# Kernel tuning notes

Measured on AMD Instinct MI355X. Metric: run time of the kernel, lower is better.

The kernel has to match this reference:

```python
import jax, jax.numpy as jnp
import numpy as np

N, M, D_IN, D_OUT = 100000, 1024, 64, 64


def setup_inputs() -> dict:
    key = jax.random.key(0)
    ks = jax.random.split(key, 8)
    # kaiming_uniform_ bound for fan_in = D_IN: sqrt(6 / fan_in) with a=sqrt(5) default? torch's
    # kaiming_uniform_ default (a=0) gives bound = sqrt(6/fan_in); exact init is irrelevant for math.
    bound = float(np.sqrt(6.0 / D_IN))
    return {
        "x": jax.random.normal(ks[0], (N, D_IN), dtype=jnp.float32),
        "neighbors": jax.random.normal(ks[1], (M, D_IN), dtype=jnp.float32),
        "Wq": jax.random.uniform(ks[2], (D_OUT, D_IN), jnp.float32, -bound, bound),
        "bq": jnp.zeros((D_OUT,), jnp.float32),
        "Wk": jax.random.uniform(ks[3], (D_OUT, D_IN), jnp.float32, -bound, bound),
        "bk": jnp.zeros((D_OUT,), jnp.float32),
        "Wv": jax.random.uniform(ks[4], (D_OUT, D_IN), jnp.float32, -bound, bound),
        "bv": jnp.zeros((D_OUT,), jnp.float32),
    }


def reference(x, neighbors, Wq, bq, Wk, bk, Wv, bv):
    # q: [N, D_OUT], k: [M, D_OUT]
    q = x @ Wq.T + bq
    k = neighbors @ Wk.T + bk
    # scores: [N, M] -- same math as sum(q[:,None,:] * k[None,:,:], axis=2) but via GEMM
    scores = q @ k.T
    attn = jax.nn.softmax(scores, axis=1)
    # attn @ neighbors: [N, D_IN], then value projection -> [N, D_OUT]
    agg = attn @ neighbors
    return agg @ Wv.T + bv
```

## Files before the change

### kernel.cpp

```cpp
#include <hip/hip_runtime.h>


#define N_ROWS 100000
#define LOG2E 1.44269504088896f
#define GATE_THR 11.5424f

typedef __attribute__((ext_vector_type(8))) _Float16 half8;
typedef __attribute__((ext_vector_type(4))) float    f32x4;

#define MFMA16(a,b,c) __builtin_amdgcn_mfma_f32_16x16x32_f16((a),(b),(c),0,0,0)

static __device__ __forceinline__ f32x4 zero4() {
    f32x4 v = {0.f, 0.f, 0.f, 0.f};
    return v;
}

__global__ __launch_bounds__(256)
void prep_kernel(const float* __restrict__ nb, const float* __restrict__ Wq,
                 const float* __restrict__ bq, const float* __restrict__ Wk,
                 unsigned short* __restrict__ GFh, unsigned short* __restrict__ GFl,
                 float* __restrict__ uW, unsigned short* __restrict__ KF,
                 unsigned short* __restrict__ VF)
{
    __shared__ __align__(16) float sm[8192];
    const int tid = threadIdx.x;
    if (blockIdx.x == 0) {
        const float4* wk4 = (const float4*)Wk;
        const float4* wq4 = (const float4*)Wq;
        float4* dk = (float4*)sm;
        float4* dq = (float4*)(sm + 4096);
        #pragma unroll
        for (int u = 0; u < 4; u++) {
            dk[u * 256 + tid] = wk4[u * 256 + tid];
            dq[u * 256 + tid] = wq4[u * 256 + tid];
        }
        __syncthreads();
        const int e2 = tid & 63, e1g = (tid >> 6) * 16;
        float g[16];
        #pragma unroll
        for (int q = 0; q < 16; q++) g[q] = 0.f;
        for (int w = 0; w < 64; w++) {
            float kv = sm[w * 64 + e2];
            const float* wqp = sm + 4096 + w * 64 + e1g;
            #pragma unroll
            for (int q = 0; q < 16; q++) g[q] = fmaf(wqp[q], kv, g[q]);
        }
        union { half8 h; uint4 u; } ph0, pl0, ph1, pl1;
        #pragma unroll
        for (int i = 0; i < 8; i++) {
            _Float16 h0 = (_Float16)g[i];
            ph0.h[i] = h0; pl0.h[i] = (_Float16)(g[i] - (float)h0);
            _Float16 h1 = (_Float16)g[8 + i];
            ph1.h[i] = h1; pl1.h[i] = (_Float16)(g[8 + i] - (float)h1);
        }
        const int mt = e2 >> 4, cc = e2 & 15;
        const int ks = tid >> 7, Q0 = 2 * ((tid >> 6) & 1);
        const int f  = mt * 2 + ks;
        *(uint4*)(GFh + (f * 64 + Q0 * 16 + cc) * 8)       = ph0.u;
        *(uint4*)(GFh + (f * 64 + (Q0 + 1) * 16 + cc) * 8) = ph1.u;
        *(uint4*)(GFl + (f * 64 + Q0 * 16 + cc) * 8)       = pl0.u;
        *(uint4*)(GFl + (f * 64 + (Q0 + 1) * 16 + cc) * 8) = pl1.u;
        if (tid < 64) {
            float uu = 0.f;
            for (int w = 0; w < 64; w++) uu = fmaf(bq[w], sm[w * 64 + tid], uu);
            uW[tid] = uu;
        }
    } else {
        const int j0 = (blockIdx.x - 1) * 64;
        const int T0 = (blockIdx.x - 1) * 2;
        {
            const int jr = tid >> 2, c0 = (tid & 3) * 16;
            const float* np = nb + (size_t)(j0 + jr) * 64 + c0;
            #pragma unroll
            for (int u = 0; u < 4; u++) {
                float4 v = *(const float4*)(np + 4 * u);
                sm[jr * 65 + c0 + 4 * u]     = v.x;
                sm[jr * 65 + c0 + 4 * u + 1] = v.y;
                sm[jr * 65 + c0 + 4 * u + 2] = v.z;
                sm[jr * 65 + c0 + 4 * u + 3] = v.w;
            }
        }
        #pragma unroll
        for (int s = 0; s < 2; s++) {
            const int slot = tid + 256 * s;
            const int tt = (slot >> 8) & 1, f = (slot >> 6) & 3, ln = slot & 63;
            const int t = f >> 1, h = f & 1, Qw = ln >> 4, cw = ln & 15;
            const int key = ((cw >> 3) & 1) * 16 + ((cw >> 2) & 1) * 8 + 4 * t + (cw & 3);
            const float* kp = nb + (size_t)((T0 + tt) * 32 + key) * 64 + h * 32 + Qw * 8;
            float b[8];
            *(float4*)b       = *(const float4*)kp;
            *(float4*)(b + 4) = *(const float4*)(kp + 4);
            union { half8 hh; uint4 u; } pk;
            #pragma unroll
            for (int i = 0; i < 8; i++) pk.hh[i] = (_Float16)b[i];
            *(uint4*)(KF + (size_t)(T0 + tt) * 2048 + f * 512 + ln * 8) = pk.u;
        }
        __syncthreads();
        #pragma unroll
        for (int s = 0; s < 2; s++) {
            const int slot = tid + 256 * s;
            const int tt = (slot >> 8) & 1, dt = (slot >> 6) & 3, ln = slot & 63;
            const int Qw = ln >> 4, cw = ln & 15;
            union { half8 hh; uint4 u; } pv;
            #pragma unroll
            for (int i = 0; i < 8; i++)
                pv.hh[i] = (_Float16)sm[(tt * 32 + Qw * 8 + i) * 65 + dt * 16 + cw];
            *(uint4*)(VF + (size_t)(T0 + tt) * 2048 + dt * 512 + ln * 8) = pv.u;
        }
    }
}

__global__ __launch_bounds__(64, 2)
void attn_kernel(const float* __restrict__ x,
                 const unsigned short* __restrict__ GFh,
                 const unsigned short* __restrict__ GFl,
                 const float* __restrict__ uW,
                 const unsigned short* __restrict__ KF,
                 const unsigned short* __restrict__ VF,
                 const float* __restrict__ Wv,
                 const float* __restrict__ bv,
                 float* __restrict__ out)
{
    __shared__ __align__(16) float slice[1088];
    const int lane = threadIdx.x & 63;
    const int Q    = lane >> 4;
    const int c    = lane & 15;
    const int rbase = blockIdx.x * 32;

    half8 qh[2][2], ql[2][2];
    #pragma unroll
    for (int rt = 0; rt < 2; rt++) {
        const int row = rbase + rt * 16 + c;
        half8 xh[2], xl[2];
        #pragma unroll
        for (int ks = 0; ks < 2; ks++) {
            const float* xp = x + (size_t)row * 64 + ks * 32 + Q * 8;
            float a[8];
            *(float4*)a       = *(const float4*)xp;
            *(float4*)(a + 4) = *(const float4*)(xp + 4);
            #pragma unroll
            for (int i = 0; i < 8; i++) {
                _Float16 h = (_Float16)a[i];
                xh[ks][i] = h;
                xl[ks][i] = (_Float16)(a[i] - (float)h);
            }
        }
        #pragma unroll
        for (int mt = 0; mt < 4; mt++) {
            f32x4 Cm = zero4();
            #pragma unroll
            for (int ks = 0; ks < 2; ks++) {
                half8 gh = *(const half8*)(GFh + ((mt * 2 + ks) * 64 + lane) * 8);
                half8 gl = *(const half8*)(GFl + ((mt * 2 + ks) * 64 + lane) * 8);
                Cm = MFMA16(gh, xh[ks], Cm);
                Cm = MFMA16(gh, xl[ks], Cm);
                Cm = MFMA16(gl, xh[ks], Cm);
            }
            *(f32x4*)(slice + c * 68 + mt * 16 + 4 * Q) = Cm;
        }
        __builtin_amdgcn_s_waitcnt(0);
        #pragma unroll
        for (int ks = 0; ks < 2; ks++) {
            const float* qp = slice + c * 68 + ks * 32 + Q * 8;
            const float* up = uW + ks * 32 + Q * 8;
            #pragma unroll
            for (int i = 0; i < 8; i++) {
                float val = (qp[i] + up[i]) * LOG2E;
                _Float16 h = (_Float16)val;
                qh[rt][ks][i] = h;
                ql[rt][ks][i] = (_Float16)(val - (float)h);
            }
        }
        __builtin_amdgcn_s_waitcnt(0);
    }

    f32x4 acc[2][4];
    #pragma unroll
    for (int qt = 0; qt < 2; qt++)
        #pragma unroll
        for (int dt = 0; dt < 4; dt++) acc[qt][dt] = zero4();
    float mrow[2] = { -3.0e38f, -3.0e38f };
    float lrow[2] = { 0.f, 0.f };

    const unsigned short* kfl = KF + lane * 8;
    const unsigned short* vfl = VF + lane * 8;
    half8 kA[4], kB[4], vA[4], vB[4];
    #pragma unroll
    for (int f = 0; f < 4; f++) {
        kA[f] = *(const half8*)(kfl + f * 512);
        kB[f] = *(const half8*)(kfl + 2048 + f * 512);
        vA[f] = *(const half8*)(vfl + f * 512);
        vB[f] = *(const half8*)(vfl + 2048 + f * 512);
    }

    #pragma unroll 1
    for (int TT = 0; TT < 16; TT++) {
        const int Tn = (TT < 15) ? (2 * TT + 2) : 30;

        f32x4 Sa[2][2], Sb[2][2];
        #pragma unroll
        for (int t = 0; t < 2; t++)
            #pragma unroll
            for (int qt = 0; qt < 2; qt++) {
                f32x4 s = MFMA16(kA[2 * t],     qh[qt][0], zero4());
                s = MFMA16(kA[2 * t + 1], qh[qt][1], s);
                s = MFMA16(kA[2 * t],     ql[qt][0], s);
                s = MFMA16(kA[2 * t + 1], ql[qt][1], s);
                Sa[t][qt] = s;
                f32x4 u = MFMA16(kB[2 * t],     qh[qt][0], zero4());
                u = MFMA16(kB[2 * t + 1], qh[qt][1], u);
                u = MFMA16(kB[2 * t],     ql[qt][0], u);
                u = MFMA16(kB[2 * t + 1], ql[qt][1], u);
                Sb[t][qt] = u;
            }
        #pragma unroll
        for (int f = 0; f < 4; f++) {
            kA[f] = *(const half8*)(kfl + (size_t)Tn * 2048 + f * 512);
            kB[f] = *(const half8*)(kfl + (size_t)(Tn + 1) * 2048 + f * 512);
        }

        float pmax[2];
        #pragma unroll
        for (int qt = 0; qt < 2; qt++) {
            float ma = fmaxf(fmaxf(fmaxf(Sa[0][qt][0], Sa[0][qt][1]),
                                   fmaxf(Sa[0][qt][2], Sa[0][qt][3])),
                             fmaxf(fmaxf(Sa[1][qt][0], Sa[1][qt][1]),
                                   fmaxf(Sa[1][qt][2], Sa[1][qt][3])));
            float mb = fmaxf(fmaxf(fmaxf(Sb[0][qt][0], Sb[0][qt][1]),
                                   fmaxf(Sb[0][qt][2], Sb[0][qt][3])),
                             fmaxf(fmaxf(Sb[1][qt][0], Sb[1][qt][1]),
                                   fmaxf(Sb[1][qt][2], Sb[1][qt][3])));
            pmax[qt] = fmaxf(ma, mb);
        }
        if (__any((pmax[0] > mrow[0] + GATE_THR) | (pmax[1] > mrow[1] + GATE_THR))) {
            #pragma unroll
            for (int qt = 0; qt < 2; qt++) {
                float cm = pmax[qt];
                cm = fmaxf(cm, __shfl_xor(cm, 16));
                cm = fmaxf(cm, __shfl_xor(cm, 32));
                const float mn = fmaxf(mrow[qt], cm);
                const float sc = __builtin_amdgcn_exp2f(mrow[qt] - mn);
                mrow[qt] = mn;
                lrow[qt] *= sc;
                #pragma unroll
                for (int dt = 0; dt < 4; dt++)
                    #pragma unroll
                    for (int r = 0; r < 4; r++) acc[qt][dt][r] *= sc;
            }
        }

        half8 pBa[2], pBb[2];
        #pragma unroll
        for (int qt = 0; qt < 2; qt++) {
            const float mref = mrow[qt];
            float ps = 0.f;
            float pa[8], pb[8];
            #pragma unroll
            for (int r = 0; r < 4; r++) {
                pa[r]     = __builtin_amdgcn_exp2f(Sa[0][qt][r] - mref);
                pa[4 + r] = __builtin_amdgcn_exp2f(Sa[1][qt][r] - mref);
                pb[r]     = __builtin_amdgcn_exp2f(Sb[0][qt][r] - mref);
                pb[4 + r] = __builtin_amdgcn_exp2f(Sb[1][qt][r] - mref);
            }
            #pragma unroll
            for (int i = 0; i < 8; i++) { ps += pa[i]; ps += pb[i]; }
            lrow[qt] += ps;
            #pragma unroll
            for (int i = 0; i < 8; i++) {
                pBa[qt][i] = (_Float16)pa[i];
                pBb[qt][i] = (_Float16)pb[i];
            }
        }
        #pragma unroll
        for (int dt = 0; dt < 4; dt++) {
            acc[0][dt] = MFMA16(vA[dt], pBa[0], acc[0][dt]);
            acc[1][dt] = MFMA16(vA[dt], pBa[1], acc[1][dt]);
            acc[0][dt] = MFMA16(vB[dt], pBb[0], acc[0][dt]);
            acc[1][dt] = MFMA16(vB[dt], pBb[1], acc[1][dt]);
        }
        #pragma unroll
        for (int d = 0; d < 4; d++) {
            vA[d] = *(const half8*)(vfl + (size_t)Tn * 2048 + d * 512);
            vB[d] = *(const half8*)(vfl + (size_t)(Tn + 1) * 2048 + d * 512);
        }
    }

    #pragma unroll
    for (int qt = 0; qt < 2; qt++) {
        float l = lrow[qt];
        l += __shfl_xor(l, 16);
        l += __shfl_xor(l, 32);
        const float rl = 1.f / l;
        #pragma unroll
        for (int dt = 0; dt < 4; dt++)
            #pragma unroll
            for (int r = 0; r < 4; r++) acc[qt][dt][r] *= rl;
    }
    half8 wf[4][2];
    #pragma unroll
    for (int mt = 0; mt < 4; mt++)
        #pragma unroll
        for (int ks = 0; ks < 2; ks++) {
            const float* wp = Wv + (size_t)(mt * 16 + c) * 64 + ks * 32 + Q * 8;
            #pragma unroll
            for (int i = 0; i < 8; i++) wf[mt][ks][i] = (_Float16)wp[i];
        }
    const int srcA = 32 * (Q & 1) + c;
    const int srcB = srcA + 16;
    const bool hi = (Q >> 1) & 1;
    f32x4 o[2][4];
    #pragma unroll
    for (int qt = 0; qt < 2; qt++) {
        half8 pe[2];
        #pragma unroll
        for (int ks = 0; ks < 2; ks++) {
            #pragma unroll
            for (int r = 0; r < 4; r++) {
                float a0 = __shfl(acc[qt][2 * ks + 0][r], srcA);
                float a1 = __shfl(acc[qt][2 * ks + 1][r], srcA);
                float b0 = __shfl(acc[qt][2 * ks + 0][r], srcB);
                float b1 = __shfl(acc[qt][2 * ks + 1][r], srcB);
                pe[ks][r]     = (_Float16)(hi ? a1 : a0);
                pe[ks][4 + r] = (_Float16)(hi ? b1 : b0);
            }
        }
        #pragma unroll
        for (int mt = 0; mt < 4; mt++) {
            f32x4 t = MFMA16(wf[mt][0], pe[0], zero4());
            o[qt][mt] = MFMA16(wf[mt][1], pe[1], t);
        }
    }
    #pragma unroll
    for (int qt = 0; qt < 2; qt++) {
        const int row = rbase + qt * 16 + c;
        #pragma unroll
        for (int mt = 0; mt < 4; mt++) {
            const float4 bf = *(const float4*)(bv + mt * 16 + 4 * Q);
            float4 vv = make_float4(o[qt][mt][0] + bf.x, o[qt][mt][1] + bf.y,
                                    o[qt][mt][2] + bf.z, o[qt][mt][3] + bf.w);
            *(float4*)(out + (size_t)row * 64 + mt * 16 + 4 * Q) = vv;
        }
    }
}

extern "C" void kernel_launch(void* const* d_in, const int* in_sizes, int n_in,
                              void* d_out, int out_size, void* d_ws, size_t ws_size,
                              hipStream_t stream)
{
    const float* x  = (const float*)d_in[0];
    const float* nb = (const float*)d_in[1];
    const float* Wq = (const float*)d_in[2];
    const float* bq = (const float*)d_in[3];
    const float* Wk = (const float*)d_in[4];
    const float* Wv = (const float*)d_in[6];
    const float* bv = (const float*)d_in[7];
    float* out = (float*)d_out;

    char* ws = (char*)d_ws;
    unsigned short* GFh = (unsigned short*)(ws);
    unsigned short* GFl = (unsigned short*)(ws + 8192);
    float*          uW  = (float*)(ws + 16384);
    unsigned short* KF  = (unsigned short*)(ws + 16640);
    unsigned short* VF  = (unsigned short*)(ws + 147712);

    prep_kernel<<<17, 256, 0, stream>>>(nb, Wq, bq, Wk, GFh, GFl, uW, KF, VF);
    const int grid = N_ROWS / 32;
    attn_kernel<<<grid, 64, 0, stream>>>(x, GFh, GFl, uW, KF, VF, Wv, bv, out);
}
```

Baseline: 150.0 us.

## Stage K/V tiles through LDS with async global_load_lds double buffering

```diff
diff --git a/kernel.cpp b/kernel.cpp
--- a/kernel.cpp
+++ b/kernel.cpp
@@ -9,10 +9,17 @@
 typedef __attribute__((ext_vector_type(4))) float    f32x4;
 
 #define MFMA16(a,b,c) __builtin_amdgcn_mfma_f32_16x16x32_f16((a),(b),(c),0,0,0)
+#define WAIT_LGKM0()  __builtin_amdgcn_s_waitcnt(0xc07f)
 
 static __device__ __forceinline__ f32x4 zero4() {
     f32x4 v = {0.f, 0.f, 0.f, 0.f};
     return v;
+}
+
+static __device__ __forceinline__ void gload16(const void* g, void* l) {
+    __builtin_amdgcn_global_load_lds(
+        (const __attribute__((address_space(1))) unsigned int*)g,
+        (__attribute__((address_space(3))) unsigned int*)l, 16, 0, 0);
 }
 
 __global__ __launch_bounds__(256)
@@ -110,7 +117,7 @@
     }
 }
 
-__global__ __launch_bounds__(64, 2)
+__global__ __launch_bounds__(128, 2)
 void attn_kernel(const float* __restrict__ x,
                  const unsigned short* __restrict__ GFh,
                  const unsigned short* __restrict__ GFl,
@@ -121,16 +128,31 @@
                  const float* __restrict__ bv,
                  float* __restrict__ out)
 {
-    __shared__ __align__(16) float slice[1088];
-    const int lane = threadIdx.x & 63;
+    __shared__ __align__(16) char smem[32768];
+    const int tid  = threadIdx.x;
+    const int lane = tid & 63;
+    const int wv   = tid >> 6;
     const int Q    = lane >> 4;
     const int c    = lane & 15;
-    const int rbase = blockIdx.x * 32;
+    const int rbase = blockIdx.x * 64 + wv * 32;
+    float* slice = (float*)(smem + 16384) + wv * 1088;
+
+    {
+        const size_t tgl = (size_t)wv * 2048 + (size_t)lane * 8;
+        char* dK = smem + wv * 4096;
+        char* dV = smem + 8192 + wv * 4096;
+        #pragma unroll
+        for (int f = 0; f < 4; f++) {
+            gload16(KF + tgl + f * 512, dK + f * 1024);
+            gload16(VF + tgl + f * 512, dV + f * 1024);
+        }
+    }
 
     half8 qh[2][2], ql[2][2];
     #pragma unroll
     for (int rt = 0; rt < 2; rt++) {
-        const int row = rbase + rt * 16 + c;
+        int row = rbase + rt * 16 + c;
+        if (row > N_ROWS - 1) row = N_ROWS - 1;
         half8 xh[2], xl[2];
         #pragma unroll
         for (int ks = 0; ks < 2; ks++) {
@@ -158,7 +180,7 @@
             }
             *(f32x4*)(slice + c * 68 + mt * 16 + 4 * Q) = Cm;
         }
-        __builtin_amdgcn_s_waitcnt(0);
+        WAIT_LGKM0();
         #pragma unroll
         for (int ks = 0; ks < 2; ks++) {
             const float* qp = slice + c * 68 + ks * 32 + Q * 8;
@@ -171,8 +193,9 @@
                 ql[rt][ks][i] = (_Float16)(val - (float)h);
             }
         }
-        __builtin_amdgcn_s_waitcnt(0);
-    }
+        WAIT_LGKM0();
+    }
+    __syncthreads();
 
     f32x4 acc[2][4];
     #pragma unroll
@@ -182,20 +205,28 @@
     float mrow[2] = { -3.0e38f, -3.0e38f };
     float lrow[2] = { 0.f, 0.f };
 
-    const unsigned short* kfl = KF + lane * 8;
-    const unsigned short* vfl = VF + lane * 8;
-    half8 kA[4], kB[4], vA[4], vB[4];
-    #pragma unroll
-    for (int f = 0; f < 4; f++) {
-        kA[f] = *(const half8*)(kfl + f * 512);
-        kB[f] = *(const half8*)(kfl + 2048 + f * 512);
-        vA[f] = *(const half8*)(vfl + f * 512);
-        vB[f] = *(const half8*)(vfl + 2048 + f * 512);
-    }
-
     #pragma unroll 1
     for (int TT = 0; TT < 16; TT++) {
-        const int Tn = (TT < 15) ? (2 * TT + 2) : 30;
+        if (TT < 15) {
+            const size_t tgl = (size_t)(2 * (TT + 1) + wv) * 2048 + (size_t)lane * 8;
+            char* base = smem + ((TT + 1) & 1) * 16384;
+            char* dK = base + wv * 4096;
+            char* dV = base + 8192 + wv * 4096;
+            #pragma unroll
+            for (int f = 0; f < 4; f++) {
+                gload16(KF + tgl + f * 512, dK + f * 1024);
+                gload16(VF + tgl + f * 512, dV + f * 1024);
+            }
+        }
+        const char* rb = smem + (TT & 1) * 16384;
+        half8 kA[4], kB[4], vA[4], vB[4];
+        #pragma unroll
+        for (int f = 0; f < 4; f++) {
+            kA[f] = *(const half8*)(rb + f * 1024 + lane * 16);
+            kB[f] = *(const half8*)(rb + 4096 + f * 1024 + lane * 16);
+            vA[f] = *(const half8*)(rb + 8192 + f * 1024 + lane * 16);
+            vB[f] = *(const half8*)(rb + 12288 + f * 1024 + lane * 16);
+        }
 
         f32x4 Sa[2][2], Sb[2][2];
         #pragma unroll
@@ -213,11 +244,6 @@
                 u = MFMA16(kB[2 * t + 1], ql[qt][1], u);
                 Sb[t][qt] = u;
             }
-        #pragma unroll
-        for (int f = 0; f < 4; f++) {
-            kA[f] = *(const half8*)(kfl + (size_t)Tn * 2048 + f * 512);
-            kB[f] = *(const half8*)(kfl + (size_t)(Tn + 1) * 2048 + f * 512);
-        }
 
         float pmax[2];
         #pragma unroll
@@ -278,11 +304,7 @@
             acc[0][dt] = MFMA16(vB[dt], pBb[0], acc[0][dt]);
             acc[1][dt] = MFMA16(vB[dt], pBb[1], acc[1][dt]);
         }
-        #pragma unroll
-        for (int d = 0; d < 4; d++) {
-            vA[d] = *(const half8*)(vfl + (size_t)Tn * 2048 + d * 512);
-            vB[d] = *(const half8*)(vfl + (size_t)(Tn + 1) * 2048 + d * 512);
-        }
+        __syncthreads();
     }
 
     #pragma unroll
@@ -333,12 +355,14 @@
     #pragma unroll
     for (int qt = 0; qt < 2; qt++) {
         const int row = rbase + qt * 16 + c;
-        #pragma unroll
-        for (int mt = 0; mt < 4; mt++) {
-            const float4 bf = *(const float4*)(bv + mt * 16 + 4 * Q);
-            float4 vv = make_float4(o[qt][mt][0] + bf.x, o[qt][mt][1] + bf.y,
-                                    o[qt][mt][2] + bf.z, o[qt][mt][3] + bf.w);
-            *(float4*)(out + (size_t)row * 64 + mt * 16 + 4 * Q) = vv;
+        if (row < N_ROWS) {
+            #pragma unroll
+            for (int mt = 0; mt < 4; mt++) {
+                const float4 bf = *(const float4*)(bv + mt * 16 + 4 * Q);
+                float4 vv = make_float4(o[qt][mt][0] + bf.x, o[qt][mt][1] + bf.y,
+                                        o[qt][mt][2] + bf.z, o[qt][mt][3] + bf.w);
+                *(float4*)(out + (size_t)row * 64 + mt * 16 + 4 * Q) = vv;
+            }
         }
     }
 }
@@ -364,6 +388,6 @@
     unsigned short* VF  = (unsigned short*)(ws + 147712);
 
     prep_kernel<<<17, 256, 0, stream>>>(nb, Wq, bq, Wk, GFh, GFl, uW, KF, VF);
-    const int grid = N_ROWS / 32;
-    attn_kernel<<<grid, 64, 0, stream>>>(x, GFh, GFl, uW, KF, VF, Wv, bv, out);
-}
+    const int grid = (N_ROWS + 63) / 64;
+    attn_kernel<<<grid, 128, 0, stream>>>(x, GFh, GFl, uW, KF, VF, Wv, bv, out);
+}
```

Result: slower. 161.7 us (+7.8%).

## Software-pipeline QK and softmax-PV per tile with single K/V buffers

Applied to the files above, without the earlier changes.

```diff
diff --git a/kernel.cpp b/kernel.cpp
--- a/kernel.cpp
+++ b/kernel.cpp
@@ -6,6 +6,7 @@
 #define GATE_THR 11.5424f
 
 typedef __attribute__((ext_vector_type(8))) _Float16 half8;
+typedef __attribute__((ext_vector_type(2))) __fp16   fp16x2;
 typedef __attribute__((ext_vector_type(4))) float    f32x4;
 
 #define MFMA16(a,b,c) __builtin_amdgcn_mfma_f32_16x16x32_f16((a),(b),(c),0,0,0)
@@ -110,7 +111,80 @@
     }
 }
 
-__global__ __launch_bounds__(64, 2)
+static __device__ __forceinline__ void load4(half8 (&dst)[4], const unsigned short* base) {
+    #pragma unroll
+    for (int f = 0; f < 4; f++) dst[f] = *(const half8*)(base + f * 512);
+}
+
+static __device__ __forceinline__ void qk_tile(
+    const half8 (&k)[4], const half8 (&qh)[2][2], const half8 (&ql)[2][2],
+    f32x4 (&S)[2][2])
+{
+    #pragma unroll
+    for (int t = 0; t < 2; t++)
+        #pragma unroll
+        for (int qt = 0; qt < 2; qt++) {
+            f32x4 s = MFMA16(k[2 * t],     qh[qt][0], zero4());
+            s = MFMA16(k[2 * t + 1], qh[qt][1], s);
+            s = MFMA16(k[2 * t],     ql[qt][0], s);
+            s = MFMA16(k[2 * t + 1], ql[qt][1], s);
+            S[t][qt] = s;
+        }
+}
+
+static __device__ __forceinline__ void sm_pv(
+    const f32x4 (&S)[2][2], const half8 (&vA)[4],
+    f32x4 (&acc)[2][4], float (&mrow)[2], float (&lrow)[2])
+{
+    float pmax[2];
+    #pragma unroll
+    for (int qt = 0; qt < 2; qt++) {
+        pmax[qt] = fmaxf(fmaxf(fmaxf(S[0][qt][0], S[0][qt][1]),
+                               fmaxf(S[0][qt][2], S[0][qt][3])),
+                         fmaxf(fmaxf(S[1][qt][0], S[1][qt][1]),
+                               fmaxf(S[1][qt][2], S[1][qt][3])));
+    }
+    if (__any((pmax[0] > mrow[0] + GATE_THR) | (pmax[1] > mrow[1] + GATE_THR))) {
+        #pragma unroll
+        for (int qt = 0; qt < 2; qt++) {
+            float cm = pmax[qt];
+            cm = fmaxf(cm, __shfl_xor(cm, 16));
+            cm = fmaxf(cm, __shfl_xor(cm, 32));
+            const float mn = fmaxf(mrow[qt], cm);
+            const float sc = __builtin_amdgcn_exp2f(mrow[qt] - mn);
+            mrow[qt] = mn;
+            lrow[qt] *= sc;
+            #pragma unroll
+            for (int dt = 0; dt < 4; dt++)
+                #pragma unroll
+                for (int r = 0; r < 4; r++) acc[qt][dt][r] *= sc;
+        }
+    }
+    union { half8 v; fp16x2 h2[4]; } pk[2];
+    #pragma unroll
+    for (int qt = 0; qt < 2; qt++) {
+        const float mref = mrow[qt];
+        float p[8]; float ps = 0.f;
+        #pragma unroll
+        for (int r = 0; r < 4; r++) {
+            p[r]     = __builtin_amdgcn_exp2f(S[0][qt][r] - mref);
+            p[4 + r] = __builtin_amdgcn_exp2f(S[1][qt][r] - mref);
+        }
+        #pragma unroll
+        for (int i = 0; i < 8; i++) ps += p[i];
+        lrow[qt] += ps;
+        #pragma unroll
+        for (int j = 0; j < 4; j++)
+            pk[qt].h2[j] = __builtin_amdgcn_cvt_pkrtz(p[2 * j], p[2 * j + 1]);
+    }
+    #pragma unroll
+    for (int dt = 0; dt < 4; dt++) {
+        acc[0][dt] = MFMA16(vA[dt], pk[0].v, acc[0][dt]);
+        acc[1][dt] = MFMA16(vA[dt], pk[1].v, acc[1][dt]);
+    }
+}
+
+__global__ __launch_bounds__(64, 3)
 void attn_kernel(const float* __restrict__ x,
                  const unsigned short* __restrict__ GFh,
                  const unsigned short* __restrict__ GFl,
@@ -184,105 +258,28 @@
 
     const unsigned short* kfl = KF + lane * 8;
     const unsigned short* vfl = VF + lane * 8;
-    half8 kA[4], kB[4], vA[4], vB[4];
-    #pragma unroll
-    for (int f = 0; f < 4; f++) {
-        kA[f] = *(const half8*)(kfl + f * 512);
-        kB[f] = *(const half8*)(kfl + 2048 + f * 512);
-        vA[f] = *(const half8*)(vfl + f * 512);
-        vB[f] = *(const half8*)(vfl + 2048 + f * 512);
-    }
+    half8 kA[4], vA[4];
+    f32x4 Sa[2][2], Sb[2][2];
+
+    load4(kA, kfl);
+    load4(vA, vfl);
+    qk_tile(kA, qh, ql, Sa);
+    load4(kA, kfl + 2048);
 
     #pragma unroll 1
     for (int TT = 0; TT < 16; TT++) {
-        const int Tn = (TT < 15) ? (2 * TT + 2) : 30;
-
-        f32x4 Sa[2][2], Sb[2][2];
-        #pragma unroll
-        for (int t = 0; t < 2; t++)
-            #pragma unroll
-            for (int qt = 0; qt < 2; qt++) {
-                f32x4 s = MFMA16(kA[2 * t],     qh[qt][0], zero4());
-                s = MFMA16(kA[2 * t + 1], qh[qt][1], s);
-                s = MFMA16(kA[2 * t],     ql[qt][0], s);
-                s = MFMA16(kA[2 * t + 1], ql[qt][1], s);
-                Sa[t][qt] = s;
-                f32x4 u = MFMA16(kB[2 * t],     qh[qt][0], zero4());
-                u = MFMA16(kB[2 * t + 1], qh[qt][1], u);
-                u = MFMA16(kB[2 * t],     ql[qt][0], u);
-                u = MFMA16(kB[2 * t + 1], ql[qt][1], u);
-                Sb[t][qt] = u;
-            }
-        #pragma unroll
-        for (int f = 0; f < 4; f++) {
-            kA[f] = *(const half8*)(kfl + (size_t)Tn * 2048 + f * 512);
-            kB[f] = *(const half8*)(kfl + (size_t)(Tn + 1) * 2048 + f * 512);
-        }
-
-        float pmax[2];
-        #pragma unroll
-        for (int qt = 0; qt < 2; qt++) {
-            float ma = fmaxf(fmaxf(fmaxf(Sa[0][qt][0], Sa[0][qt][1]),
-                                   fmaxf(Sa[0][qt][2], Sa[0][qt][3])),
-                             fmaxf(fmaxf(Sa[1][qt][0], Sa[1][qt][1]),
-                                   fmaxf(Sa[1][qt][2], Sa[1][qt][3])));
-            float mb = fmaxf(fmaxf(fmaxf(Sb[0][qt][0], Sb[0][qt][1]),
-                                   fmaxf(Sb[0][qt][2], Sb[0][qt][3])),
-                             fmaxf(fmaxf(Sb[1][qt][0], Sb[1][qt][1]),
-                                   fmaxf(Sb[1][qt][2], Sb[1][qt][3])));
-            pmax[qt] = fmaxf(ma, mb);
-        }
-        if (__any((pmax[0] > mrow[0] + GATE_THR) | (pmax[1] > mrow[1] + GATE_THR))) {
-            #pragma unroll
-            for (int qt = 0; qt < 2; qt++) {
-                float cm = pmax[qt];
-                cm = fmaxf(cm, __shfl_xor(cm, 16));
-                cm = fmaxf(cm, __shfl_xor(cm, 32));
-                const float mn = fmaxf(mrow[qt], cm);
-                const float sc = __builtin_amdgcn_exp2f(mrow[qt] - mn);
-                mrow[qt] = mn;
-                lrow[qt] *= sc;
-                #pragma unroll
-                for (int dt = 0; dt < 4; dt++)
-                    #pragma unroll
-                    for (int r = 0; r < 4; r++) acc[qt][dt][r] *= sc;
-            }
-        }
-
-        half8 pBa[2], pBb[2];
-        #pragma unroll
-        for (int qt = 0; qt < 2; qt++) {
-            const float mref = mrow[qt];
-            float ps = 0.f;
-            float pa[8], pb[8];
-            #pragma unroll
-            for (int r = 0; r < 4; r++) {
-                pa[r]     = __builtin_amdgcn_exp2f(Sa[0][qt][r] - mref);
-                pa[4 + r] = __builtin_amdgcn_exp2f(Sa[1][qt][r] - mref);
-                pb[r]     = __builtin_amdgcn_exp2f(Sb[0][qt][r] - mref);
-                pb[4 + r] = __builtin_amdgcn_exp2f(Sb[1][qt][r] - mref);
-            }
-            #pragma unroll
-            for (int i = 0; i < 8; i++) { ps += pa[i]; ps += pb[i]; }
-            lrow[qt] += ps;
-            #pragma unroll
-            for (int i = 0; i < 8; i++) {
-                pBa[qt][i] = (_Float16)pa[i];
-                pBb[qt][i] = (_Float16)pb[i];
-            }
-        }
-        #pragma unroll
-        for (int dt = 0; dt < 4; dt++) {
-            acc[0][dt] = MFMA16(vA[dt], pBa[0], acc[0][dt]);
-            acc[1][dt] = MFMA16(vA[dt], pBa[1], acc[1][dt]);
-            acc[0][dt] = MFMA16(vB[dt], pBb[0], acc[0][dt]);
-            acc[1][dt] = MFMA16(vB[dt], pBb[1], acc[1][dt]);
-        }
-        #pragma unroll
-        for (int d = 0; d < 4; d++) {
-            vA[d] = *(const half8*)(vfl + (size_t)Tn * 2048 + d * 512);
-            vB[d] = *(const half8*)(vfl + (size_t)(Tn + 1) * 2048 + d * 512);
-        }
+        qk_tile(kA, qh, ql, Sb);
+        {   int Tn = 2 * TT + 2; if (Tn > 31) Tn = 31;
+            load4(kA, kfl + (size_t)Tn * 2048); }
+        sm_pv(Sa, vA, acc, mrow, lrow);
+        {   int Tn = 2 * TT + 1; if (Tn > 31) Tn = 31;
+            load4(vA, vfl + (size_t)Tn * 2048); }
+        qk_tile(kA, qh, ql, Sa);
+        {   int Tn = 2 * TT + 3; if (Tn > 31) Tn = 31;
+            load4(kA, kfl + (size_t)Tn * 2048); }
+        sm_pv(Sb, vA, acc, mrow, lrow);
+        {   int Tn = 2 * TT + 2; if (Tn > 31) Tn = 31;
+            load4(vA, vfl + (size_t)Tn * 2048); }
     }
 
     #pragma unroll
```

After: 152.4 us. Within noise of the previous version (+1.6%).
